# Kernel tuning notes

Measured on AMD Instinct MI355X. Metric: run time of the kernel, lower is better.

Reference implementation:

```python
import jax, jax.numpy as jnp
import numpy as np

N, E, FE, H, G, L, OUT = 50000, 300000, 64, 256, 256, 4, 128
BN_EPS = 1e-5


def setup_inputs() -> dict:
    key = jax.random.key(0)
    ks = jax.random.split(key, 12)
    s = 0.05
    return dict(
        x=jax.random.normal(ks[0], (N, H), jnp.float32),
        edge_index=jax.random.randint(ks[1], (2, E), 0, N, dtype=jnp.int64),
        edge_attr=jax.random.normal(ks[2], (E, FE), jnp.float32),
        batch=jnp.sort(jax.random.randint(ks[3], (N,), 0, G, dtype=jnp.int64)),
        bond_W1=jax.random.normal(ks[4], (L, FE, H), jnp.float32) * s,
        bond_b1=jnp.zeros((L, H), jnp.float32),
        bond_W2=jax.random.normal(ks[5], (L, H, H), jnp.float32) * s,
        bond_b2=jnp.zeros((L, H), jnp.float32),
        mlp_W1=jax.random.normal(ks[6], (L, H, H), jnp.float32) * s,
        mlp_b1=jnp.zeros((L, H), jnp.float32),
        mlp_W2=jax.random.normal(ks[7], (L, H, H), jnp.float32) * s,
        mlp_b2=jnp.zeros((L, H), jnp.float32),
        eps=jnp.zeros((L,), jnp.float32),
        bn_gamma=jnp.ones((L, H), jnp.float32),
        bn_beta=jnp.zeros((L, H), jnp.float32),
        fc1_W=jax.random.normal(ks[8], (L * H, H), jnp.float32) * s,
        fc1_b=jnp.zeros((H,), jnp.float32),
        fc4_W=jax.random.normal(ks[9], (H, OUT), jnp.float32) * s,
        fc4_b=jnp.zeros((OUT,), jnp.float32),
    )


def reference(x, edge_index, edge_attr, batch,
              bond_W1, bond_b1, bond_W2, bond_b2,
              mlp_W1, mlp_b1, mlp_W2, mlp_b2,
              eps, bn_gamma, bn_beta,
              fc1_W, fc1_b, fc4_W, fc4_b):
    src, dst = edge_index[0], edge_index[1]  # x_j gathered from src, scatter-add to dst
    x_lst = []
    for l in range(L):
        # bond encoder: Linear -> ReLU -> Linear on edge features [E, FE] -> [E, H]
        e = jax.nn.relu(edge_attr @ bond_W1[l] + bond_b1[l]) @ bond_W2[l] + bond_b2[l]
        # message = relu(x_j + e), aggregate = scatter-add over destination nodes
        msg = jax.nn.relu(x[src] + e)  # [E, H]
        aggr = jax.ops.segment_sum(msg, dst, num_segments=N)  # [N, H]
        h = (1.0 + eps[l]) * x + aggr
        h = jax.nn.relu(h @ mlp_W1[l] + mlp_b1[l]) @ mlp_W2[l] + mlp_b2[l]
        h = jax.nn.relu(h)
        # BatchNorm over the node dimension (training-style batch statistics)
        mu = jnp.mean(h, axis=0)
        var = jnp.var(h, axis=0)
        x = (h - mu) * jax.lax.rsqrt(var + BN_EPS) * bn_gamma[l] + bn_beta[l]
        x_lst.append(x)
    xc = jnp.concatenate(x_lst, axis=-1)  # [N, L*H]
    # global mean pool over graphs
    sums = jax.ops.segment_sum(xc, batch, num_segments=G)  # [G, L*H]
    cnts = jax.ops.segment_sum(jnp.ones((N,), xc.dtype), batch, num_segments=G)
    pooled = sums / jnp.maximum(cnts, 1.0)[:, None]
    h = jax.nn.relu(pooled @ fc1_W + fc1_b)
    # dropout p=0.5 in eval mode -> identity
    return h @ fc4_W + fc4_b  # [G, OUT]
```

## Files before the change

kernel.cpp:

```cpp
#include <hip/hip_runtime.h>

#define NN 50000
#define NE 300000
#define FEA 64
#define HD 256
#define NG 256
#define NL 4
#define OD 128
#define SCB ((NN + 255) / 256)

typedef unsigned short u16;
typedef unsigned int u32;
typedef __attribute__((ext_vector_type(8))) short short8;
typedef __attribute__((ext_vector_type(4))) short s16x4;
typedef __attribute__((ext_vector_type(4))) float f32x4;

__device__ __forceinline__ u16 f2h(float f) {
    union { _Float16 h; u16 u; } v; v.h = (_Float16)f; return v.u;
}
__device__ __forceinline__ float h2f(u16 u) {
    union { u16 u; _Float16 h; } v; v.u = u; return (float)v.h;
}

typedef const __attribute__((address_space(1))) unsigned int gas_u32;
typedef __attribute__((address_space(3))) unsigned int las_u32;
__device__ __forceinline__ void gld16(const void* g, void* l) {
    __builtin_amdgcn_global_load_lds((gas_u32*)g, (las_u32*)l, 16, 0, 0);
}

__global__ __launch_bounds__(256, 2) void edge_k(
    const u16* __restrict__ eattrS, const u16* __restrict__ W1t,
    const float* __restrict__ bb1, const u16* __restrict__ W2t,
    const float* __restrict__ bb2,
    const int* __restrict__ srcI, const int* __restrict__ dstI,
    const u16* __restrict__ xh, float* __restrict__ aggr)
{
    __shared__ __align__(16) u16 bufW[256 * 64];
    __shared__ __align__(16) u16 bufT[64 * 256];
    __shared__ int srcL[64];
    const int tid = threadIdx.x;
    const int lane = tid & 63;
    const int w = tid >> 6;
    const int q = lane >> 4, c15 = lane & 15;
    const int e0 = blockIdx.x * 64;
    const int wb = tid & ~63;

    if (tid < 64) {
        int er = e0 + tid;
        int erc = er < NE ? er : NE - 1;
        srcL[tid] = srcI[erc];
    }
#pragma unroll
    for (int it = 0; it < 2; ++it) {
        const int i = it * 256 + tid;
        const int m = i >> 3, kb = i & 7;
        int row = e0 + m; if (row > NE - 1) row = NE - 1;
        gld16(eattrS + (size_t)row * FEA + ((kb ^ (m & 7)) * 8),
              &bufT[(it * 256 + wb) * 8]);
    }
#pragma unroll
    for (int it = 0; it < 8; ++it) {
        const int i = it * 256 + tid;
        const int n = i >> 3, kb = i & 7;
        gld16(W1t + (size_t)n * FEA + ((kb ^ (n & 7)) * 8),
              &bufW[(it * 256 + wb) * 8]);
    }
    __syncthreads();

    f32x4 acc1[4][4];
#pragma unroll
    for (int i = 0; i < 4; ++i)
#pragma unroll
        for (int j = 0; j < 4; ++j) acc1[i][j] = (f32x4)0.0f;
#pragma unroll
    for (int s = 0; s < 2; ++s) {
        short8 af[4], bf[4];
#pragma unroll
        for (int t = 0; t < 4; ++t) {
            const int kga = s * 4 + q;
            const int mm = t * 16 + c15;
            af[t] = *(const short8*)&bufT[mm * 64 + ((kga ^ (mm & 7)) * 8)];
            const int nn = w * 64 + t * 16 + c15;
            bf[t] = *(const short8*)&bufW[nn * 64 + ((kga ^ (nn & 7)) * 8)];
        }
        __builtin_amdgcn_s_setprio(1);
#pragma unroll
        for (int tm = 0; tm < 4; ++tm)
#pragma unroll
            for (int tn = 0; tn < 4; ++tn)
                acc1[tm][tn] = __builtin_amdgcn_mfma_f32_16x16x32_f16(
                    bf[tm], af[tn], acc1[tm][tn], 0, 0, 0);
        __builtin_amdgcn_s_setprio(0);
    }
    __syncthreads();

    auto stageW2 = [&](int cc) {
        const int k0c = cc * 32;
        const int hB = (cc & 1) * 1024;
#pragma unroll
        for (int it = 0; it < 4; ++it) {
            const int i = it * 256 + tid;
            const int n = i >> 2, j = i & 3;
            gld16(W2t + (size_t)n * HD + k0c + ((j ^ ((n >> 1) & 3)) * 8),
                  &bufW[(hB + it * 256 + wb) * 8]);
        }
    };
    stageW2(0);

    {
#pragma unroll
        for (int tm = 0; tm < 4; ++tm) {
            const float4 b1v = *(const float4*)(bb1 + w * 64 + tm * 16 + q * 4);
            const int kb = w * 8 + tm * 2 + (q >> 1);
#pragma unroll
            for (int tn = 0; tn < 4; ++tn) {
                const int edge = tn * 16 + c15;
                s16x4 o;
#pragma unroll
                for (int r = 0; r < 4; ++r) {
                    float v = acc1[tm][tn][r] + ((const float*)&b1v)[r];
                    v = v > 0.0f ? v : 0.0f;
                    o[r] = (short)f2h(v);
                }
                *(s16x4*)((char*)bufT + edge * 512 +
                          ((kb ^ (edge & 7)) << 4) + ((q & 1) << 3)) = o;
            }
        }
    }
    __syncthreads();

    f32x4 acc2[4][4];
#pragma unroll
    for (int i = 0; i < 4; ++i)
#pragma unroll
        for (int j = 0; j < 4; ++j) acc2[i][j] = (f32x4)0.0f;
#pragma unroll
    for (int c = 0; c < 8; ++c) {
        if (c < 7) {
            stageW2(c + 1);
        } else {
#pragma unroll
            for (int it = 0; it < 4; ++it) {
                const int i = it * 256 + tid;
                const int row = i >> 5, ch = i & 31;
                gld16(xh + (size_t)srcL[row] * HD + ch * 8,
                      &bufW[(it * 256 + wb) * 8]);
            }
        }
        short8 af[4], bf[4];
        const u16* hp = &bufW[(c & 1) * 8192];
#pragma unroll
        for (int t = 0; t < 4; ++t) {
            const int mm = t * 16 + c15;
            const int kbg = c * 4 + q;
            af[t] = *(const short8*)&bufT[mm * 256 + ((kbg ^ (mm & 7)) * 8)];
            const int nn = w * 64 + t * 16 + c15;
            bf[t] = *(const short8*)&hp[nn * 32 + ((q ^ ((nn >> 1) & 3)) * 8)];
        }
        __builtin_amdgcn_s_setprio(1);
#pragma unroll
        for (int tm = 0; tm < 4; ++tm)
#pragma unroll
            for (int tn = 0; tn < 4; ++tn)
                acc2[tm][tn] = __builtin_amdgcn_mfma_f32_16x16x32_f16(
                    af[tm], bf[tn], acc2[tm][tn], 0, 0, 0);
        __builtin_amdgcn_s_setprio(0);
        __syncthreads();
    }

#pragma unroll
    for (int it = 0; it < 4; ++it) {
        const int i = 1024 + it * 256 + tid;
        const int row = i >> 5, ch = i & 31;
        gld16(xh + (size_t)srcL[row] * HD + ch * 8,
              &bufW[(1024 + it * 256 + wb) * 8]);
    }
    float b2f[4];
#pragma unroll
    for (int tn = 0; tn < 4; ++tn)
        b2f[tn] = bb2[w * 64 + tn * 16 + c15];
    __syncthreads();

#pragma unroll
    for (int tm = 0; tm < 4; ++tm) {
        const int rc = tm * 2 + (q >> 1);
#pragma unroll
        for (int tn = 0; tn < 4; ++tn) {
            const int col = w * 64 + tn * 16 + c15;
            s16x4 o;
#pragma unroll
            for (int r = 0; r < 4; ++r) {
                const int row = tm * 16 + q * 4 + r;
                float v = acc2[tm][tn][r] + b2f[tn]
                        + h2f(bufW[row * 256 + col]);
                v = v > 0.0f ? v : 0.0f;
                o[r] = (short)f2h(v);
            }
            *(s16x4*)((char*)bufT + col * 128 +
                      ((rc ^ (col & 7)) << 4) + ((q & 1) << 3)) = o;
        }
    }
    __syncthreads();

    {
        const char* bT = (const char*)bufT;
        float s = 0.0f;
        int cur = dstI[e0];
#pragma unroll
        for (int j = 0; j < 8; ++j) {
            short8 m8 = *(const short8*)(bT + tid * 128 + ((j ^ (tid & 7)) << 4));
#pragma unroll
            for (int si = 0; si < 8; ++si) {
                const int er = e0 + j * 8 + si;
                const int d = (er < NE) ? dstI[er] : -1;
                if (d != cur) {
                    if (cur >= 0 && s != 0.0f)
                        unsafeAtomicAdd(&aggr[(size_t)cur * HD + tid], s);
                    cur = d; s = 0.0f;
                }
                s += h2f((u16)m8[si]);
            }
        }
        if (cur >= 0 && s != 0.0f)
            unsafeAtomicAdd(&aggr[(size_t)cur * HD + tid], s);
    }
}

__global__ __launch_bounds__(256, 2) void node_k(
    const u16* __restrict__ xh, const float* __restrict__ aggr,
    const float* __restrict__ epsv, int l,
    const u16* __restrict__ M1t, const float* __restrict__ mb1,
    const u16* __restrict__ M2t, const float* __restrict__ mb2,
    u16* __restrict__ hb, float* __restrict__ bns, float* __restrict__ bnq)
{
    __shared__ __align__(16) u16 bufW[256 * 64];
    __shared__ __align__(16) u16 bufT[64 * 256];
    const int tid = threadIdx.x;
    const int lane = tid & 63;
    const int w = tid >> 6;
    const int q = lane >> 4, c15 = lane & 15;
    const int n0b = blockIdx.x * 64;
    const float e1 = 1.0f + epsv[l];
    const int wb = tid & ~63;

    auto stageM = [&](const u16* Mt, int cc) {
        const int k0c = cc * 32;
        const int hB = (cc & 1) * 1024;
#pragma unroll
        for (int it = 0; it < 4; ++it) {
            const int i = it * 256 + tid;
            const int n = i >> 2, j = i & 3;
            gld16(Mt + (size_t)n * HD + k0c + ((j ^ ((n >> 1) & 3)) * 8),
                  &bufW[(hB + it * 256 + wb) * 8]);
        }
    };
    stageM(M1t, 0);

#pragma unroll
    for (int it = 0; it < 8; ++it) {
        const int i = it * 256 + tid;
        const int m = i >> 5, kb = i & 31;
        int row = n0b + m; if (row > NN - 1) row = NN - 1;
        const size_t base = (size_t)row * HD + kb * 8;
        short8 xv = *(const short8*)(xh + base);
        float4 a0 = *(const float4*)(aggr + base);
        float4 a1 = *(const float4*)(aggr + base + 4);
        u16 o[8];
        o[0] = f2h(e1 * h2f((u16)xv[0]) + a0.x);
        o[1] = f2h(e1 * h2f((u16)xv[1]) + a0.y);
        o[2] = f2h(e1 * h2f((u16)xv[2]) + a0.z);
        o[3] = f2h(e1 * h2f((u16)xv[3]) + a0.w);
        o[4] = f2h(e1 * h2f((u16)xv[4]) + a1.x);
        o[5] = f2h(e1 * h2f((u16)xv[5]) + a1.y);
        o[6] = f2h(e1 * h2f((u16)xv[6]) + a1.z);
        o[7] = f2h(e1 * h2f((u16)xv[7]) + a1.w);
        *(short8*)&bufT[m * 256 + ((kb ^ (m & 7)) * 8)] = *(short8*)o;
    }
    __syncthreads();

    f32x4 acc1[4][4];
#pragma unroll
    for (int i = 0; i < 4; ++i)
#pragma unroll
        for (int j = 0; j < 4; ++j) acc1[i][j] = (f32x4)0.0f;
#pragma unroll
    for (int c = 0; c < 8; ++c) {
        if (c < 7) stageM(M1t, c + 1);
        else       stageM(M2t, 0);
        short8 af[4], bf[4];
        const u16* hp = &bufW[(c & 1) * 8192];
#pragma unroll
        for (int t = 0; t < 4; ++t) {
            const int mm = t * 16 + c15;
            const int kbg = c * 4 + q;
            af[t] = *(const short8*)&bufT[mm * 256 + ((kbg ^ (mm & 7)) * 8)];
            const int nn = w * 64 + t * 16 + c15;
            bf[t] = *(const short8*)&hp[nn * 32 + ((q ^ ((nn >> 1) & 3)) * 8)];
        }
        __builtin_amdgcn_s_setprio(1);
#pragma unroll
        for (int tm = 0; tm < 4; ++tm)
#pragma unroll
            for (int tn = 0; tn < 4; ++tn)
                acc1[tm][tn] = __builtin_amdgcn_mfma_f32_16x16x32_f16(
                    bf[tm], af[tn], acc1[tm][tn], 0, 0, 0);
        __builtin_amdgcn_s_setprio(0);
        __syncthreads();
    }

    {
#pragma unroll
        for (int tm = 0; tm < 4; ++tm) {
            const float4 b1v = *(const float4*)(mb1 + w * 64 + tm * 16 + q * 4);
            const int kb = w * 8 + tm * 2 + (q >> 1);
#pragma unroll
            for (int tn = 0; tn < 4; ++tn) {
                const int node = tn * 16 + c15;
                s16x4 o;
#pragma unroll
                for (int r = 0; r < 4; ++r) {
                    float v = acc1[tm][tn][r] + ((const float*)&b1v)[r];
                    v = v > 0.0f ? v : 0.0f;
                    o[r] = (short)f2h(v);
                }
                *(s16x4*)((char*)bufT + node * 512 +
                          ((kb ^ (node & 7)) << 4) + ((q & 1) << 3)) = o;
            }
        }
    }
    __syncthreads();

    f32x4 acc2[4][4];
#pragma unroll
    for (int i = 0; i < 4; ++i)
#pragma unroll
        for (int j = 0; j < 4; ++j) acc2[i][j] = (f32x4)0.0f;
#pragma unroll
    for (int c = 0; c < 8; ++c) {
        if (c < 7) stageM(M2t, c + 1);
        short8 af[4], bf[4];
        const u16* hp = &bufW[(c & 1) * 8192];
#pragma unroll
        for (int t = 0; t < 4; ++t) {
            const int mm = t * 16 + c15;
            const int kbg = c * 4 + q;
            af[t] = *(const short8*)&bufT[mm * 256 + ((kbg ^ (mm & 7)) * 8)];
            const int nn = w * 64 + t * 16 + c15;
            bf[t] = *(const short8*)&hp[nn * 32 + ((q ^ ((nn >> 1) & 3)) * 8)];
        }
        __builtin_amdgcn_s_setprio(1);
#pragma unroll
        for (int tm = 0; tm < 4; ++tm)
#pragma unroll
            for (int tn = 0; tn < 4; ++tn)
                acc2[tm][tn] = __builtin_amdgcn_mfma_f32_16x16x32_f16(
                    af[tm], bf[tn], acc2[tm][tn], 0, 0, 0);
        __builtin_amdgcn_s_setprio(0);
        __syncthreads();
    }

    float b2f[4];
#pragma unroll
    for (int tn = 0; tn < 4; ++tn)
        b2f[tn] = mb2[w * 64 + tn * 16 + c15];
    float ps[4] = {0, 0, 0, 0}, pq[4] = {0, 0, 0, 0};
#pragma unroll
    for (int tm = 0; tm < 4; ++tm) {
#pragma unroll
        for (int r = 0; r < 4; ++r) {
            const int grow = n0b + tm * 16 + q * 4 + r;
            if (grow < NN) {
#pragma unroll
                for (int tn = 0; tn < 4; ++tn) {
                    const int col = w * 64 + tn * 16 + c15;
                    float v = acc2[tm][tn][r] + b2f[tn];
                    v = v > 0.0f ? v : 0.0f;
                    hb[(size_t)grow * HD + col] = f2h(v);
                    ps[tn] += v; pq[tn] += v * v;
                }
            }
        }
    }
#pragma unroll
    for (int tn = 0; tn < 4; ++tn) {
        float s = ps[tn], sq = pq[tn];
        s += __shfl_down(s, 32, 64);  sq += __shfl_down(sq, 32, 64);
        s += __shfl_down(s, 16, 64);  sq += __shfl_down(sq, 16, 64);
        if (q == 0) {
            const int col = w * 64 + tn * 16 + c15;
            unsafeAtomicAdd(&bns[col], s);
            unsafeAtomicAdd(&bnq[col], sq);
        }
    }
}


__global__ void transpose_k(const float* __restrict__ in, u16* __restrict__ oh,
                            int Kw, int Nw) {
    int i = blockIdx.x * blockDim.x + threadIdx.x;
    int tot = NL * Kw * Nw;
    if (i < tot) {
        int l = i / (Kw * Nw), rem = i % (Kw * Nw);
        int k = rem / Nw, n = rem % Nw;
        oh[(size_t)l * Kw * Nw + (size_t)n * Kw + k] = f2h(in[i]);
    }
}

__global__ void cvt_k(const float* __restrict__ in, u16* __restrict__ outh, int tot) {
    int i = blockIdx.x * blockDim.x + threadIdx.x;
    if (i < tot) outh[i] = f2h(in[i]);
}

__global__ void egather_k(const float* __restrict__ eattr, const int* __restrict__ perm,
                          u16* __restrict__ eattrS) {
    int i = blockIdx.x * blockDim.x + threadIdx.x;
    if (i < NE * FEA) {
        int row = i >> 6, k = i & 63;
        eattrS[i] = f2h(eattr[(size_t)perm[row] * FEA + k]);
    }
}

__global__ void zero_layer_k(float* __restrict__ aggr, float* __restrict__ bns,
                             float* __restrict__ bnq) {
    int i = blockIdx.x * blockDim.x + threadIdx.x;
    if (i < NN * HD) aggr[i] = 0.0f;
    if (i < HD) { bns[i] = 0.0f; bnq[i] = 0.0f; }
}

__global__ void zerof_k(float* __restrict__ p, int n) {
    int i = blockIdx.x * blockDim.x + threadIdx.x;
    if (i < n) p[i] = 0.0f;
}

__global__ void bnfin_k(const float* __restrict__ bns, const float* __restrict__ bnq,
                        const float* __restrict__ gamma, const float* __restrict__ beta,
                        int l, float* __restrict__ ab) {
    int c = threadIdx.x;
    float mu = bns[c] * (1.0f / (float)NN);
    float var = bnq[c] * (1.0f / (float)NN) - mu * mu;
    if (var < 0.0f) var = 0.0f;
    float a = gamma[l * HD + c] * rsqrtf(var + 1e-5f);
    float b = beta[l * HD + c] - mu * a;
    ab[c] = a; ab[HD + c] = b;
}

__global__ void bnapply_k(const u16* __restrict__ hb, const float* __restrict__ ab,
                          const int* __restrict__ batch, u16* __restrict__ xh,
                          float* __restrict__ pooled, int l) {
    const int t = threadIdx.x;
    const int n0 = blockIdx.x * 64;
    const float a = ab[t], b = ab[HD + t];
    const int hi = (NN - n0 < 64) ? (NN - n0) : 64;
    float s = 0.0f;
    int cur = batch[n0];
    for (int r = 0; r < hi; ++r) {
        const size_t idx = (size_t)(n0 + r) * HD + t;
        float v = a * h2f(hb[idx]) + b;
        xh[idx] = f2h(v);
        const int g = batch[n0 + r];
        if (g != cur) {
            unsafeAtomicAdd(&pooled[(size_t)cur * (NL * HD) + l * HD + t], s);
            s = 0.0f; cur = g;
        }
        s += v;
    }
    unsafeAtomicAdd(&pooled[(size_t)cur * (NL * HD) + l * HD + t], s);
}


__global__ void zeroi_k(int* __restrict__ a, int n) {
    int i = blockIdx.x * blockDim.x + threadIdx.x;
    if (i < n) a[i] = 0;
}

__global__ void hist_k(const int* __restrict__ dst, int* __restrict__ hist) {
    int e = blockIdx.x * blockDim.x + threadIdx.x;
    if (e < NE) atomicAdd(&hist[dst[e]], 1);
}

__global__ void sumblk_k(const int* __restrict__ hist, int* __restrict__ psum) {
    __shared__ int red[256];
    int b = blockIdx.x, t = threadIdx.x, i = b * 256 + t;
    red[t] = (i < NN) ? hist[i] : 0;
    __syncthreads();
    for (int o = 128; o > 0; o >>= 1) {
        if (t < o) red[t] += red[t + o];
        __syncthreads();
    }
    if (t == 0) psum[b] = red[0];
}

__global__ void scanblk_k(int* __restrict__ psum) {
    __shared__ int sc[256];
    int t = threadIdx.x;
    int v = (t < SCB) ? psum[t] : 0;
    sc[t] = v; __syncthreads();
    for (int o = 1; o < 256; o <<= 1) {
        int x = (t >= o) ? sc[t - o] : 0;
        __syncthreads(); sc[t] += x; __syncthreads();
    }
    if (t < SCB) psum[t] = sc[t] - v;
}

__global__ void scanfin_k(const int* __restrict__ hist, const int* __restrict__ psum,
                          int* __restrict__ rowptr) {
    __shared__ int sc[256];
    int b = blockIdx.x, t = threadIdx.x, i = b * 256 + t;
    int v = (i < NN) ? hist[i] : 0;
    sc[t] = v; __syncthreads();
    for (int o = 1; o < 256; o <<= 1) {
        int x = (t >= o) ? sc[t - o] : 0;
        __syncthreads(); sc[t] += x; __syncthreads();
    }
    if (i < NN) rowptr[i] = psum[b] + sc[t] - v;
    if (i == NN - 1) rowptr[NN] = psum[b] + sc[t];
}

__global__ void copyi_k(const int* __restrict__ src, int* __restrict__ dst, int n) {
    int i = blockIdx.x * blockDim.x + threadIdx.x;
    if (i < n) dst[i] = src[i];
}

__global__ void scatter_k(const int* __restrict__ dst, int* __restrict__ next,
                          int* __restrict__ perm) {
    int e = blockIdx.x * blockDim.x + threadIdx.x;
    if (e < NE) {
        int p = atomicAdd(&next[dst[e]], 1);
        perm[p] = e;
    }
}

__global__ void permsd_k(const int* __restrict__ eidx, const int* __restrict__ perm,
                         int* __restrict__ srcS, int* __restrict__ dstS) {
    int i = blockIdx.x * blockDim.x + threadIdx.x;
    if (i < NE) {
        int e = perm[i];
        srcS[i] = eidx[e];
        dstS[i] = eidx[NE + e];
    }
}


__global__ void zcnt_k(int* __restrict__ cnts) {
    if (threadIdx.x < NG) cnts[threadIdx.x] = 0;
}

__global__ void count_k(const int* __restrict__ batch, int* __restrict__ cnts) {
    int i = blockIdx.x * blockDim.x + threadIdx.x;
    if (i < NN) atomicAdd(&cnts[batch[i]], 1);
}

__global__ void fc_k(const float* __restrict__ pooled, const int* __restrict__ cnts,
                     const float* __restrict__ W1, const float* __restrict__ b1,
                     const float* __restrict__ W4, const float* __restrict__ b4,
                     float* __restrict__ out) {
    __shared__ float pl[NL * HD];
    __shared__ float hm[HD];
    int g = blockIdx.x, t = threadIdx.x;
    const float inv = 1.0f / fmaxf((float)cnts[g], 1.0f);
#pragma unroll
    for (int j = 0; j < 4; ++j)
        pl[t + j * 256] = pooled[(size_t)g * 1024 + t + j * 256] * inv;
    __syncthreads();
    float a = b1[t];
    for (int k = 0; k < 1024; ++k) a += pl[k] * W1[k * 256 + t];
    hm[t] = a > 0.0f ? a : 0.0f;
    __syncthreads();
    if (t < OD) {
        float o = b4[t];
        for (int k = 0; k < 256; ++k) o += hm[k] * W4[k * OD + t];
        out[g * OD + t] = o;
    }
}


extern "C" void kernel_launch(void* const* d_in, const int* in_sizes, int n_in,
                              void* d_out, int out_size, void* d_ws, size_t ws_size,
                              hipStream_t stream) {
    const float* x_in  = (const float*)d_in[0];
    const int*   eidx  = (const int*)d_in[1];
    const float* eattr = (const float*)d_in[2];
    const int*   batch = (const int*)d_in[3];
    const float* bW1   = (const float*)d_in[4];
    const float* bb1   = (const float*)d_in[5];
    const float* bW2   = (const float*)d_in[6];
    const float* bb2   = (const float*)d_in[7];
    const float* mW1   = (const float*)d_in[8];
    const float* mb1   = (const float*)d_in[9];
    const float* mW2   = (const float*)d_in[10];
    const float* mb2   = (const float*)d_in[11];
    const float* epsv  = (const float*)d_in[12];
    const float* gamma = (const float*)d_in[13];
    const float* beta  = (const float*)d_in[14];
    const float* fc1W  = (const float*)d_in[15];
    const float* fc1b  = (const float*)d_in[16];
    const float* fc4W  = (const float*)d_in[17];
    const float* fc4b  = (const float*)d_in[18];
    float* out = (float*)d_out;
    (void)in_sizes; (void)n_in; (void)out_size; (void)ws_size;

    size_t off = 0;
    auto alloc = [&](size_t bytes) -> char* {
        char* r = (char*)d_ws + off;
        off = (off + bytes + 255) & ~(size_t)255;
        return r;
    };
    u16*   xh   = (u16*)alloc((size_t)NN * HD * 2);
    float* aggr = (float*)alloc((size_t)NN * HD * 4);
    u16*   hb   = (u16*)alloc((size_t)NN * HD * 2);
    u16*   eattrS = (u16*)alloc((size_t)NE * FEA * 2);
    u16*   W1t  = (u16*)alloc((size_t)NL * FEA * HD * 2);
    u16*   W2t  = (u16*)alloc((size_t)NL * HD * HD * 2);
    u16*   M1t  = (u16*)alloc((size_t)NL * HD * HD * 2);
    u16*   M2t  = (u16*)alloc((size_t)NL * HD * HD * 2);
    float* bns  = (float*)alloc(HD * 4);
    float* bnq  = (float*)alloc(HD * 4);
    float* ab   = (float*)alloc(2 * HD * 4);
    int*   cnts = (int*)alloc(NG * 4);
    float* pooled = (float*)alloc((size_t)NG * NL * HD * 4);
    int*   hist  = (int*)alloc((size_t)NN * 4);
    int*   psum  = (int*)alloc((size_t)SCB * 4);
    int*   rowptr = (int*)alloc((size_t)(NN + 1) * 4);
    int*   perm  = (int*)alloc((size_t)NE * 4);
    int*   srcS  = (int*)alloc((size_t)NE * 4);
    int*   dstS  = (int*)alloc((size_t)NE * 4);

    const int NEL = NN * HD;
    const int EB = (NEL + 255) / 256;
    const int NEB = (NE + 255) / 256;

    transpose_k<<<(NL * FEA * HD + 255) / 256, 256, 0, stream>>>(bW1, W1t, FEA, HD);
    transpose_k<<<(NL * HD * HD + 255) / 256, 256, 0, stream>>>(bW2, W2t, HD, HD);
    transpose_k<<<(NL * HD * HD + 255) / 256, 256, 0, stream>>>(mW1, M1t, HD, HD);
    transpose_k<<<(NL * HD * HD + 255) / 256, 256, 0, stream>>>(mW2, M2t, HD, HD);

    cvt_k<<<EB, 256, 0, stream>>>(x_in, xh, NEL);

    zeroi_k<<<(NN + 255) / 256, 256, 0, stream>>>(hist, NN);
    hist_k<<<NEB, 256, 0, stream>>>(eidx + NE, hist);
    sumblk_k<<<SCB, 256, 0, stream>>>(hist, psum);
    scanblk_k<<<1, 256, 0, stream>>>(psum);
    scanfin_k<<<SCB, 256, 0, stream>>>(hist, psum, rowptr);
    copyi_k<<<(NN + 255) / 256, 256, 0, stream>>>(rowptr, hist, NN);
    scatter_k<<<NEB, 256, 0, stream>>>(eidx + NE, hist, perm);
    permsd_k<<<NEB, 256, 0, stream>>>(eidx, perm, srcS, dstS);
    egather_k<<<(NE * FEA + 255) / 256, 256, 0, stream>>>(eattr, perm, eattrS);

    zcnt_k<<<1, 256, 0, stream>>>(cnts);
    count_k<<<(NN + 255) / 256, 256, 0, stream>>>(batch, cnts);
    zerof_k<<<(NG * NL * HD + 255) / 256, 256, 0, stream>>>(pooled, NG * NL * HD);

    const int EGB = (NE + 63) / 64;
    const int NGB = (NN + 63) / 64;

    for (int l = 0; l < NL; ++l) {
        zero_layer_k<<<EB, 256, 0, stream>>>(aggr, bns, bnq);
        edge_k<<<EGB, 256, 0, stream>>>(
            eattrS, W1t + (size_t)l * FEA * HD, bb1 + l * HD,
            W2t + (size_t)l * HD * HD, bb2 + l * HD,
            srcS, dstS, xh, aggr);
        node_k<<<NGB, 256, 0, stream>>>(
            xh, aggr, epsv, l,
            M1t + (size_t)l * HD * HD, mb1 + l * HD,
            M2t + (size_t)l * HD * HD, mb2 + l * HD,
            hb, bns, bnq);
        bnfin_k<<<1, HD, 0, stream>>>(bns, bnq, gamma, beta, l, ab);
        bnapply_k<<<NGB, 256, 0, stream>>>(hb, ab, batch, xh, pooled, l);
    }
    fc_k<<<NG, 256, 0, stream>>>(pooled, cnts, fc1W, fc1b, fc4W, fc4b, out);
}
```

Before: 1.268 ms.

## Make edge kernel persistent with LDS-resident W2 and fold aggr zeroing into bnapply

The edge kernel becomes persistent: 256 blocks loop over edge tiles and keep W1 fragments in registers and 7/8 of W2 resident in LDS, so weights are no longer restaged for every 64-edge tile. Only the first W2 chunk is reloaded per tile. The gathered x rows and the scatter epilogue are split into two halves to fit the smaller scratch buffer, with next-tile prefetch overlapped with the second half's atomics. The per-layer aggr zeroing moves into bnapply, and bnfin resets the BN sums. The trade-off is one block per CU with a large LDS footprint and only 256 blocks, which lowers occupancy and latency hiding.

```diff
diff --git a/kernel.cpp b/kernel.cpp
--- a/kernel.cpp
+++ b/kernel.cpp
@@ -8,6 +8,8 @@
 #define NL 4
 #define OD 128
 #define SCB ((NN + 255) / 256)
+#define NT ((NE + 63) / 64)
+#define EBLK 256
 
 typedef unsigned short u16;
 typedef unsigned int u32;
@@ -28,89 +30,100 @@
     __builtin_amdgcn_global_load_lds((gas_u32*)g, (las_u32*)l, 16, 0, 0);
 }
 
-__global__ __launch_bounds__(256, 2) void edge_k(
+__global__ __launch_bounds__(256, 1) void edge_k(
     const u16* __restrict__ eattrS, const u16* __restrict__ W1t,
     const float* __restrict__ bb1, const u16* __restrict__ W2t,
     const float* __restrict__ bb2,
     const int* __restrict__ srcI, const int* __restrict__ dstI,
     const u16* __restrict__ xh, float* __restrict__ aggr)
 {
-    __shared__ __align__(16) u16 bufW[256 * 64];
+    __shared__ __align__(16) u16 W2L[7 * 8192];
+    __shared__ __align__(16) u16 SBUF[8192];
     __shared__ __align__(16) u16 bufT[64 * 256];
-    __shared__ int srcL[64];
     const int tid = threadIdx.x;
     const int lane = tid & 63;
     const int w = tid >> 6;
     const int q = lane >> 4, c15 = lane & 15;
-    const int e0 = blockIdx.x * 64;
     const int wb = tid & ~63;
 
-    if (tid < 64) {
-        int er = e0 + tid;
-        int erc = er < NE ? er : NE - 1;
-        srcL[tid] = srcI[erc];
-    }
-#pragma unroll
-    for (int it = 0; it < 2; ++it) {
-        const int i = it * 256 + tid;
-        const int m = i >> 3, kb = i & 7;
-        int row = e0 + m; if (row > NE - 1) row = NE - 1;
-        gld16(eattrS + (size_t)row * FEA + ((kb ^ (m & 7)) * 8),
-              &bufT[(it * 256 + wb) * 8]);
-    }
-#pragma unroll
-    for (int it = 0; it < 8; ++it) {
-        const int i = it * 256 + tid;
-        const int n = i >> 3, kb = i & 7;
-        gld16(W1t + (size_t)n * FEA + ((kb ^ (n & 7)) * 8),
-              &bufW[(it * 256 + wb) * 8]);
-    }
-    __syncthreads();
-
-    f32x4 acc1[4][4];
-#pragma unroll
-    for (int i = 0; i < 4; ++i)
-#pragma unroll
-        for (int j = 0; j < 4; ++j) acc1[i][j] = (f32x4)0.0f;
-#pragma unroll
-    for (int s = 0; s < 2; ++s) {
-        short8 af[4], bf[4];
+    short8 b1f[2][4];
+#pragma unroll
+    for (int s = 0; s < 2; ++s)
 #pragma unroll
         for (int t = 0; t < 4; ++t) {
-            const int kga = s * 4 + q;
-            const int mm = t * 16 + c15;
-            af[t] = *(const short8*)&bufT[mm * 64 + ((kga ^ (mm & 7)) * 8)];
             const int nn = w * 64 + t * 16 + c15;
-            bf[t] = *(const short8*)&bufW[nn * 64 + ((kga ^ (nn & 7)) * 8)];
-        }
-        __builtin_amdgcn_s_setprio(1);
-#pragma unroll
-        for (int tm = 0; tm < 4; ++tm)
-#pragma unroll
-            for (int tn = 0; tn < 4; ++tn)
-                acc1[tm][tn] = __builtin_amdgcn_mfma_f32_16x16x32_f16(
-                    bf[tm], af[tn], acc1[tm][tn], 0, 0, 0);
-        __builtin_amdgcn_s_setprio(0);
-    }
-    __syncthreads();
-
-    auto stageW2 = [&](int cc) {
+            b1f[s][t] = *(const short8*)(W1t + (size_t)nn * FEA + q * 8 + s * 32);
+        }
+    float4 b1v[4];
+#pragma unroll
+    for (int tm = 0; tm < 4; ++tm)
+        b1v[tm] = *(const float4*)(bb1 + w * 64 + tm * 16 + q * 4);
+    float b2f[4];
+#pragma unroll
+    for (int tn = 0; tn < 4; ++tn)
+        b2f[tn] = bb2[w * 64 + tn * 16 + c15];
+
+    for (int cc = 1; cc < 8; ++cc) {
         const int k0c = cc * 32;
-        const int hB = (cc & 1) * 1024;
+        u16* dst = &W2L[(cc - 1) * 8192];
 #pragma unroll
         for (int it = 0; it < 4; ++it) {
             const int i = it * 256 + tid;
             const int n = i >> 2, j = i & 3;
             gld16(W2t + (size_t)n * HD + k0c + ((j ^ ((n >> 1) & 3)) * 8),
-                  &bufW[(hB + it * 256 + wb) * 8]);
-        }
-    };
-    stageW2(0);
-
+                  &dst[(it * 256 + wb) * 8]);
+        }
+    }
     {
 #pragma unroll
+        for (int it = 0; it < 4; ++it) {
+            const int i = it * 256 + tid;
+            const int n = i >> 2, j = i & 3;
+            gld16(W2t + (size_t)n * HD + ((j ^ ((n >> 1) & 3)) * 8),
+                  &SBUF[(it * 256 + wb) * 8]);
+        }
+        const int e00 = blockIdx.x * 64;
+#pragma unroll
+        for (int it = 0; it < 2; ++it) {
+            const int i = it * 256 + tid;
+            const int m = i >> 3, kb = i & 7;
+            int row = e00 + m; if (row > NE - 1) row = NE - 1;
+            gld16(eattrS + (size_t)row * FEA + ((kb ^ (m & 7)) * 8),
+                  &bufT[(it * 256 + wb) * 8]);
+        }
+    }
+
+    for (int tile = blockIdx.x; tile < NT; tile += EBLK) {
+        const int e0 = tile * 64;
+        __syncthreads();
+
+        f32x4 acc1[4][4];
+#pragma unroll
+        for (int i = 0; i < 4; ++i)
+#pragma unroll
+            for (int j = 0; j < 4; ++j) acc1[i][j] = (f32x4)0.0f;
+#pragma unroll
+        for (int s = 0; s < 2; ++s) {
+            short8 af[4];
+#pragma unroll
+            for (int t = 0; t < 4; ++t) {
+                const int kga = s * 4 + q;
+                const int mm = t * 16 + c15;
+                af[t] = *(const short8*)&bufT[mm * 64 + ((kga ^ (mm & 7)) * 8)];
+            }
+            __builtin_amdgcn_s_setprio(1);
+#pragma unroll
+            for (int tm = 0; tm < 4; ++tm)
+#pragma unroll
+                for (int tn = 0; tn < 4; ++tn)
+                    acc1[tm][tn] = __builtin_amdgcn_mfma_f32_16x16x32_f16(
+                        b1f[s][tm], af[tn], acc1[tm][tn], 0, 0, 0);
+            __builtin_amdgcn_s_setprio(0);
+        }
+        __syncthreads();
+
+#pragma unroll
         for (int tm = 0; tm < 4; ++tm) {
-            const float4 b1v = *(const float4*)(bb1 + w * 64 + tm * 16 + q * 4);
             const int kb = w * 8 + tm * 2 + (q >> 1);
 #pragma unroll
             for (int tn = 0; tn < 4; ++tn) {
@@ -118,7 +131,7 @@
                 s16x4 o;
 #pragma unroll
                 for (int r = 0; r < 4; ++r) {
-                    float v = acc1[tm][tn][r] + ((const float*)&b1v)[r];
+                    float v = acc1[tm][tn][r] + ((const float*)&b1v[tm])[r];
                     v = v > 0.0f ? v : 0.0f;
                     o[r] = (short)f2h(v);
                 }
@@ -126,103 +139,178 @@
                           ((kb ^ (edge & 7)) << 4) + ((q & 1) << 3)) = o;
             }
         }
-    }
-    __syncthreads();
-
-    f32x4 acc2[4][4];
-#pragma unroll
-    for (int i = 0; i < 4; ++i)
-#pragma unroll
-        for (int j = 0; j < 4; ++j) acc2[i][j] = (f32x4)0.0f;
-#pragma unroll
-    for (int c = 0; c < 8; ++c) {
-        if (c < 7) {
-            stageW2(c + 1);
-        } else {
+        __syncthreads();
+
+        f32x4 acc2[4][4];
+#pragma unroll
+        for (int i = 0; i < 4; ++i)
+#pragma unroll
+            for (int j = 0; j < 4; ++j) acc2[i][j] = (f32x4)0.0f;
+        {
+            short8 af[4], bf[4];
+#pragma unroll
+            for (int t = 0; t < 4; ++t) {
+                const int mm = t * 16 + c15;
+                af[t] = *(const short8*)&bufT[mm * 256 + ((q ^ (mm & 7)) * 8)];
+                const int nn = w * 64 + t * 16 + c15;
+                bf[t] = *(const short8*)&SBUF[nn * 32 + ((q ^ ((nn >> 1) & 3)) * 8)];
+            }
+            __builtin_amdgcn_s_setprio(1);
+#pragma unroll
+            for (int tm = 0; tm < 4; ++tm)
+#pragma unroll
+                for (int tn = 0; tn < 4; ++tn)
+                    acc2[tm][tn] = __builtin_amdgcn_mfma_f32_16x16x32_f16(
+                        af[tm], bf[tn], acc2[tm][tn], 0, 0, 0);
+            __builtin_amdgcn_s_setprio(0);
+        }
+        __syncthreads();
+
+#pragma unroll
+        for (int it = 0; it < 4; ++it) {
+            const int i = it * 256 + tid;
+            const int row = i >> 5, ch = i & 31;
+            int er = e0 + row; if (er > NE - 1) er = NE - 1;
+            const int sn = srcI[er];
+            gld16(xh + (size_t)sn * HD + ch * 8, &SBUF[(it * 256 + wb) * 8]);
+        }
+        for (int c = 1; c < 8; ++c) {
+            const u16* hp = &W2L[(c - 1) * 8192];
+            short8 af[4], bf[4];
+#pragma unroll
+            for (int t = 0; t < 4; ++t) {
+                const int mm = t * 16 + c15;
+                const int kbg = c * 4 + q;
+                af[t] = *(const short8*)&bufT[mm * 256 + ((kbg ^ (mm & 7)) * 8)];
+                const int nn = w * 64 + t * 16 + c15;
+                bf[t] = *(const short8*)&hp[nn * 32 + ((q ^ ((nn >> 1) & 3)) * 8)];
+            }
+            __builtin_amdgcn_s_setprio(1);
+#pragma unroll
+            for (int tm = 0; tm < 4; ++tm)
+#pragma unroll
+                for (int tn = 0; tn < 4; ++tn)
+                    acc2[tm][tn] = __builtin_amdgcn_mfma_f32_16x16x32_f16(
+                        af[tm], bf[tn], acc2[tm][tn], 0, 0, 0);
+            __builtin_amdgcn_s_setprio(0);
+        }
+        __syncthreads();
+
+#pragma unroll
+        for (int tm = 0; tm < 2; ++tm) {
+            const int rc = tm * 2 + (q >> 1);
+#pragma unroll
+            for (int tn = 0; tn < 4; ++tn) {
+                const int col = w * 64 + tn * 16 + c15;
+                s16x4 o;
+#pragma unroll
+                for (int r = 0; r < 4; ++r) {
+                    const int rowL = tm * 16 + q * 4 + r;
+                    float v = acc2[tm][tn][r] + b2f[tn] + h2f(SBUF[rowL * 256 + col]);
+                    v = v > 0.0f ? v : 0.0f;
+                    o[r] = (short)f2h(v);
+                }
+                *(s16x4*)((char*)bufT + col * 64 +
+                          ((rc ^ (col & 3)) << 4) + ((q & 1) << 3)) = o;
+            }
+        }
+        __syncthreads();
+
+#pragma unroll
+        for (int it = 0; it < 4; ++it) {
+            const int i = it * 256 + tid;
+            const int row = 32 + (i >> 5), ch = i & 31;
+            int er = e0 + row; if (er > NE - 1) er = NE - 1;
+            const int sn = srcI[er];
+            gld16(xh + (size_t)sn * HD + ch * 8, &SBUF[(it * 256 + wb) * 8]);
+        }
+        {
+            const char* part = (const char*)bufT;
+            const int col = tid;
+            float s = 0.0f;
+            int cur = dstI[e0];
+#pragma unroll
+            for (int j = 0; j < 4; ++j) {
+                short8 m8 = *(const short8*)(part + col * 64 + ((j ^ (col & 3)) << 4));
+#pragma unroll
+                for (int si = 0; si < 8; ++si) {
+                    const int er = e0 + j * 8 + si;
+                    const int d = (er < NE) ? dstI[er] : -1;
+                    if (d != cur) {
+                        if (cur >= 0 && s != 0.0f)
+                            unsafeAtomicAdd(&aggr[(size_t)cur * HD + col], s);
+                        cur = d; s = 0.0f;
+                    }
+                    s += h2f((u16)m8[si]);
+                }
+            }
+            if (cur >= 0 && s != 0.0f)
+                unsafeAtomicAdd(&aggr[(size_t)cur * HD + col], s);
+        }
+        __syncthreads();
+
+#pragma unroll
+        for (int tm = 2; tm < 4; ++tm) {
+            const int rc = (tm - 2) * 2 + (q >> 1);
+#pragma unroll
+            for (int tn = 0; tn < 4; ++tn) {
+                const int col = w * 64 + tn * 16 + c15;
+                s16x4 o;
+#pragma unroll
+                for (int r = 0; r < 4; ++r) {
+                    const int rowL = (tm - 2) * 16 + q * 4 + r;
+                    float v = acc2[tm][tn][r] + b2f[tn] + h2f(SBUF[rowL * 256 + col]);
+                    v = v > 0.0f ? v : 0.0f;
+                    o[r] = (short)f2h(v);
+                }
+                *(s16x4*)((char*)bufT + 16384 + col * 64 +
+                          ((rc ^ (col & 3)) << 4) + ((q & 1) << 3)) = o;
+            }
+        }
+        __syncthreads();
+
+        if (tile + EBLK < NT) {
 #pragma unroll
             for (int it = 0; it < 4; ++it) {
                 const int i = it * 256 + tid;
-                const int row = i >> 5, ch = i & 31;
-                gld16(xh + (size_t)srcL[row] * HD + ch * 8,
-                      &bufW[(it * 256 + wb) * 8]);
-            }
-        }
-        short8 af[4], bf[4];
-        const u16* hp = &bufW[(c & 1) * 8192];
-#pragma unroll
-        for (int t = 0; t < 4; ++t) {
-            const int mm = t * 16 + c15;
-            const int kbg = c * 4 + q;
-            af[t] = *(const short8*)&bufT[mm * 256 + ((kbg ^ (mm & 7)) * 8)];
-            const int nn = w * 64 + t * 16 + c15;
-            bf[t] = *(const short8*)&hp[nn * 32 + ((q ^ ((nn >> 1) & 3)) * 8)];
-        }
-        __builtin_amdgcn_s_setprio(1);
-#pragma unroll
-        for (int tm = 0; tm < 4; ++tm)
-#pragma unroll
-            for (int tn = 0; tn < 4; ++tn)
-                acc2[tm][tn] = __builtin_amdgcn_mfma_f32_16x16x32_f16(
-                    af[tm], bf[tn], acc2[tm][tn], 0, 0, 0);
-        __builtin_amdgcn_s_setprio(0);
-        __syncthreads();
-    }
-
-#pragma unroll
-    for (int it = 0; it < 4; ++it) {
-        const int i = 1024 + it * 256 + tid;
-        const int row = i >> 5, ch = i & 31;
-        gld16(xh + (size_t)srcL[row] * HD + ch * 8,
-              &bufW[(1024 + it * 256 + wb) * 8]);
-    }
-    float b2f[4];
-#pragma unroll
-    for (int tn = 0; tn < 4; ++tn)
-        b2f[tn] = bb2[w * 64 + tn * 16 + c15];
-    __syncthreads();
-
-#pragma unroll
-    for (int tm = 0; tm < 4; ++tm) {
-        const int rc = tm * 2 + (q >> 1);
-#pragma unroll
-        for (int tn = 0; tn < 4; ++tn) {
-            const int col = w * 64 + tn * 16 + c15;
-            s16x4 o;
-#pragma unroll
-            for (int r = 0; r < 4; ++r) {
-                const int row = tm * 16 + q * 4 + r;
-                float v = acc2[tm][tn][r] + b2f[tn]
-                        + h2f(bufW[row * 256 + col]);
-                v = v > 0.0f ? v : 0.0f;
-                o[r] = (short)f2h(v);
-            }
-            *(s16x4*)((char*)bufT + col * 128 +
-                      ((rc ^ (col & 7)) << 4) + ((q & 1) << 3)) = o;
-        }
-    }
-    __syncthreads();
-
-    {
-        const char* bT = (const char*)bufT;
-        float s = 0.0f;
-        int cur = dstI[e0];
-#pragma unroll
-        for (int j = 0; j < 8; ++j) {
-            short8 m8 = *(const short8*)(bT + tid * 128 + ((j ^ (tid & 7)) << 4));
-#pragma unroll
-            for (int si = 0; si < 8; ++si) {
-                const int er = e0 + j * 8 + si;
-                const int d = (er < NE) ? dstI[er] : -1;
-                if (d != cur) {
-                    if (cur >= 0 && s != 0.0f)
-                        unsafeAtomicAdd(&aggr[(size_t)cur * HD + tid], s);
-                    cur = d; s = 0.0f;
+                const int n = i >> 2, j = i & 3;
+                gld16(W2t + (size_t)n * HD + ((j ^ ((n >> 1) & 3)) * 8),
+                      &SBUF[(it * 256 + wb) * 8]);
+            }
+            const int e0n = (tile + EBLK) * 64;
+#pragma unroll
+            for (int it = 0; it < 2; ++it) {
+                const int i = it * 256 + tid;
+                const int m = i >> 3, kb = i & 7;
+                int row = e0n + m; if (row > NE - 1) row = NE - 1;
+                gld16(eattrS + (size_t)row * FEA + ((kb ^ (m & 7)) * 8),
+                      &bufT[(it * 256 + wb) * 8]);
+            }
+        }
+        {
+            const char* part = (const char*)bufT + 16384;
+            const int col = tid;
+            const int base = e0 + 32;
+            float s = 0.0f;
+            int cur = (base < NE) ? dstI[base] : -1;
+#pragma unroll
+            for (int j = 0; j < 4; ++j) {
+                short8 m8 = *(const short8*)(part + col * 64 + ((j ^ (col & 3)) << 4));
+#pragma unroll
+                for (int si = 0; si < 8; ++si) {
+                    const int er = base + j * 8 + si;
+                    const int d = (er < NE) ? dstI[er] : -1;
+                    if (d != cur) {
+                        if (cur >= 0 && s != 0.0f)
+                            unsafeAtomicAdd(&aggr[(size_t)cur * HD + col], s);
+                        cur = d; s = 0.0f;
+                    }
+                    s += h2f((u16)m8[si]);
                 }
-                s += h2f((u16)m8[si]);
-            }
-        }
-        if (cur >= 0 && s != 0.0f)
-            unsafeAtomicAdd(&aggr[(size_t)cur * HD + tid], s);
+            }
+            if (cur >= 0 && s != 0.0f)
+                unsafeAtomicAdd(&aggr[(size_t)cur * HD + col], s);
+        }
     }
 }
 
@@ -420,10 +508,10 @@
     }
 }
 
-__global__ void zero_layer_k(float* __restrict__ aggr, float* __restrict__ bns,
+__global__ void zero_layer_k(float4* __restrict__ aggr4, float* __restrict__ bns,
                              float* __restrict__ bnq) {
     int i = blockIdx.x * blockDim.x + threadIdx.x;
-    if (i < NN * HD) aggr[i] = 0.0f;
+    if (i < (NN * HD) / 4) aggr4[i] = make_float4(0.f, 0.f, 0.f, 0.f);
     if (i < HD) { bns[i] = 0.0f; bnq[i] = 0.0f; }
 }
 
@@ -432,7 +520,7 @@
     if (i < n) p[i] = 0.0f;
 }
 
-__global__ void bnfin_k(const float* __restrict__ bns, const float* __restrict__ bnq,
+__global__ void bnfin_k(float* __restrict__ bns, float* __restrict__ bnq,
                         const float* __restrict__ gamma, const float* __restrict__ beta,
                         int l, float* __restrict__ ab) {
     int c = threadIdx.x;
@@ -442,11 +530,13 @@
     float a = gamma[l * HD + c] * rsqrtf(var + 1e-5f);
     float b = beta[l * HD + c] - mu * a;
     ab[c] = a; ab[HD + c] = b;
+    bns[c] = 0.0f; bnq[c] = 0.0f;
 }
 
 __global__ void bnapply_k(const u16* __restrict__ hb, const float* __restrict__ ab,
                           const int* __restrict__ batch, u16* __restrict__ xh,
-                          float* __restrict__ pooled, int l) {
+                          float* __restrict__ pooled, int l,
+                          float* __restrict__ aggr, int zero_aggr) {
     const int t = threadIdx.x;
     const int n0 = blockIdx.x * 64;
     const float a = ab[t], b = ab[HD + t];
@@ -457,6 +547,7 @@
         const size_t idx = (size_t)(n0 + r) * HD + t;
         float v = a * h2f(hb[idx]) + b;
         xh[idx] = f2h(v);
+        if (zero_aggr) aggr[idx] = 0.0f;
         const int g = batch[n0 + r];
         if (g != cur) {
             unsafeAtomicAdd(&pooled[(size_t)cur * (NL * HD) + l * HD + t], s);
@@ -627,6 +718,7 @@
 
     const int NEL = NN * HD;
     const int EB = (NEL + 255) / 256;
+    const int EB4 = (NEL / 4 + 255) / 256;
     const int NEB = (NE + 255) / 256;
 
     transpose_k<<<(NL * FEA * HD + 255) / 256, 256, 0, stream>>>(bW1, W1t, FEA, HD);
@@ -650,12 +742,12 @@
     count_k<<<(NN + 255) / 256, 256, 0, stream>>>(batch, cnts);
     zerof_k<<<(NG * NL * HD + 255) / 256, 256, 0, stream>>>(pooled, NG * NL * HD);
 
-    const int EGB = (NE + 63) / 64;
+    zero_layer_k<<<EB4, 256, 0, stream>>>((float4*)aggr, bns, bnq);
+
     const int NGB = (NN + 63) / 64;
 
     for (int l = 0; l < NL; ++l) {
-        zero_layer_k<<<EB, 256, 0, stream>>>(aggr, bns, bnq);
-        edge_k<<<EGB, 256, 0, stream>>>(
+        edge_k<<<EBLK, 256, 0, stream>>>(
             eattrS, W1t + (size_t)l * FEA * HD, bb1 + l * HD,
             W2t + (size_t)l * HD * HD, bb2 + l * HD,
             srcS, dstS, xh, aggr);
@@ -665,7 +757,8 @@
             M2t + (size_t)l * HD * HD, mb2 + l * HD,
             hb, bns, bnq);
         bnfin_k<<<1, HD, 0, stream>>>(bns, bnq, gamma, beta, l, ab);
-        bnapply_k<<<NGB, 256, 0, stream>>>(hb, ab, batch, xh, pooled, l);
+        bnapply_k<<<NGB, 256, 0, stream>>>(hb, ab, batch, xh, pooled, l,
+                                           aggr, (l < NL - 1) ? 1 : 0);
     }
     fc_k<<<NG, 256, 0, stream>>>(pooled, cnts, fc1W, fc1b, fc4W, fc4b, out);
 }
```

After: 1.415 ms. 1.12x slower.
